# Kernel optimization log

Hardware: AMD Instinct MI355X
Metric: run time of the kernel (lower is better)

The kernel has to match this reference:

```python
import jax, jax.numpy as jnp
import numpy as np

WIDTH = 256
FREQS = 10
INPUT_WIDTH = 3 + 3 * 2 * FREQS  # 63


def embed_point(point, freqs):
    # point: [N, 3] -> [N, 3*(1+2*freqs)]
    linear = point[..., None]                                  # [N, 3, 1]
    scales = jnp.exp2(jnp.arange(freqs, dtype=point.dtype))    # [freqs]
    angles = linear * scales                                   # [N, 3, freqs]
    emb = jnp.concatenate((linear, jnp.sin(angles), jnp.cos(angles)), axis=-1)
    return emb.reshape(*point.shape[:-1], 3 * (1 + 2 * freqs))


def _xavier(key, fan_in, fan_out):
    limit = jnp.sqrt(6.0 / (fan_in + fan_out)).astype(jnp.float32)
    return jax.random.uniform(key, (fan_in, fan_out), jnp.float32, -limit, limit)


def setup_inputs() -> dict:
    key = jax.random.key(0)
    keys = jax.random.split(key, 20)
    N = 524288
    point = jax.random.normal(keys[0], (N, 3), dtype=jnp.float32)
    dims = [
        (INPUT_WIDTH, WIDTH), (WIDTH, WIDTH), (WIDTH, WIDTH), (WIDTH, WIDTH),
        (WIDTH, WIDTH), (WIDTH + INPUT_WIDTH, WIDTH), (WIDTH, WIDTH),
        (WIDTH, WIDTH), (WIDTH, 4),
    ]
    inp = {"point": point}
    for i, (fi, fo) in enumerate(dims):
        inp[f"w{i}"] = _xavier(keys[1 + i], fi, fo)
        inp[f"b{i}"] = jnp.zeros((fo,), dtype=jnp.float32)
    return inp


def reference(point, w0, b0, w1, b1, w2, b2, w3, b3, w4, b4,
              w5, b5, w6, b6, w7, b7, w8, b8):
    inp = embed_point(point, FREQS)                 # [N, 63]
    x = jax.nn.relu(inp @ w0 + b0)
    x = jax.nn.relu(x @ w1 + b1)
    x = jax.nn.relu(x @ w2 + b2)
    x = jax.nn.relu(x @ w3 + b3)
    x = jax.nn.relu(x @ w4 + b4)
    x = jax.nn.relu(jnp.concatenate((x, inp), -1) @ w5 + b5)  # skip concat
    x = jax.nn.relu(x @ w6 + b6)
    x = jax.nn.relu(x @ w7 + b7)
    return x @ w8 + b8                              # [N, 4]
```

## Files before the change

### kernel.cpp

```cpp
#include <hip/hip_runtime.h>
#include <math.h>


typedef __attribute__((ext_vector_type(8))) short short8;
typedef __attribute__((ext_vector_type(4))) float f32x4;

struct WPtrs { const float* w[8]; };
struct BPtrs { const float* b[8]; };

#define INV2PI 0.15915494309189533577f

#define ACT_PITCH 264
#define EMB_PITCH 72

#define PK_L0 0
#define PK_L1 16384
#define PK_L2 81920
#define PK_L3 147456
#define PK_L4 212992
#define PK_L5 278528
#define PK_L6 360448
#define PK_L7 425984
#define PK_W8 491520
#define PK_TOTAL 495616

__device__ __forceinline__ unsigned short f2bf(float v) {
  unsigned u = __float_as_uint(v);
  u = u + 0x7fffu + ((u >> 16) & 1u);
  return (unsigned short)(u >> 16);
}
__device__ __forceinline__ float bf_lo(unsigned u) { return __uint_as_float(u << 16); }
__device__ __forceinline__ float bf_hi(unsigned u) { return __uint_as_float(u & 0xffff0000u); }

__device__ __forceinline__ unsigned cvtpk(float a, float b) {
#if __has_builtin(__builtin_amdgcn_cvt_pk_bf16_f32)
  typedef __attribute__((ext_vector_type(2))) __bf16 bf16x2_t;
  bf16x2_t r = __builtin_amdgcn_cvt_pk_bf16_f32(a, b);
  return __builtin_bit_cast(unsigned, r);
#else
  unsigned ua = __float_as_uint(a);
  ua += 0x7fffu + ((ua >> 16) & 1u);
  unsigned ub = __float_as_uint(b);
  ub += 0x7fffu + ((ub >> 16) & 1u);
#if __has_builtin(__builtin_amdgcn_perm)
  return __builtin_amdgcn_perm(ub, ua, 0x07060302u);
#else
  return (ua >> 16) | (ub & 0xffff0000u);
#endif
#endif
}

__device__ __forceinline__ float fractf_(float x) {
#if __has_builtin(__builtin_amdgcn_fract_f32)
  return __builtin_amdgcn_fract_f32(x);
#else
  return x - floorf(x);
#endif
}
__device__ __forceinline__ float sin_rev(float rev) {
#if __has_builtin(__builtin_amdgcn_sinf)
  return __builtin_amdgcn_sinf(rev);
#else
  return __sinf(rev * 6.283185307179586f);
#endif
}

__device__ __forceinline__ float embval(int f, float c0, float c1, float c2,
                                        float x0, float x1, float x2) {
  if (f >= 63) return 0.0f;
  int d = (f >= 21 ? 1 : 0) + (f >= 42 ? 1 : 0);
  int r = f - d * 21;
  float c = (d == 0) ? c0 : (d == 1 ? c1 : c2);
  float x = (d == 0) ? x0 : (d == 1 ? x1 : x2);
  bool isc = r > 10;
  int e = isc ? (r - 11) : (r - 1);
  float rev = fractf_(ldexpf(x, e) + (isc ? 0.25f : 0.0f));
  float s = sin_rev(rev);
  return (r == 0) ? c : s;
}

__device__ __forceinline__ f32x4 mfma16(short8 a, short8 b, f32x4 c) {
  return __builtin_amdgcn_mfma_f32_16x16x32_bf16(a, b, c, 0, 0, 0);
}

__global__ void pack_weights(WPtrs W, const float* __restrict__ w8,
                             unsigned short* __restrict__ out) {
  int idx = blockIdx.x * 256 + threadIdx.x;
  if (idx >= PK_TOTAL) return;
  float v;
  if (idx >= PK_W8) {
    int t = idx - PK_W8;
    int j = t >> 8, k = t & 255;
    v = (j < 4) ? w8[k * 4 + j] : 0.0f;
  } else {
    int e = idx & 31;
    int blk = idx >> 5;
    int kkg = blk >> 8;
    int ch = blk & 255;
    int l, kk0;
    if      (kkg < 2)  { l = 0; kk0 = 0;  }
    else if (kkg < 10) { l = 1; kk0 = 2;  }
    else if (kkg < 18) { l = 2; kk0 = 10; }
    else if (kkg < 26) { l = 3; kk0 = 18; }
    else if (kkg < 34) { l = 4; kk0 = 26; }
    else if (kkg < 44) { l = 5; kk0 = 34; }
    else if (kkg < 52) { l = 6; kk0 = 44; }
    else               { l = 7; kk0 = 52; }
    int k = (kkg - kk0) * 32 + e;
    const int realK[8] = {63, 256, 256, 256, 256, 319, 256, 256};
    v = (k < realK[l]) ? W.w[l][k * 256 + ch] : 0.0f;
  }
  out[idx] = f2bf(v);
}

template <int KKA, int PA, int KKB, bool RB>
__device__ __forceinline__ void do_layer(
    const unsigned short* srcA, const unsigned short* srcB,
    const unsigned short* __restrict__ wblk,
    const float* __restrict__ bias,
    unsigned short* dst, int w, int quad, int l16) {
  f32x4 acc[4][4];
#pragma unroll
  for (int mt = 0; mt < 4; ++mt) {
    f32x4 bv = *reinterpret_cast<const f32x4*>(bias + w * 64 + mt * 16 + quad * 4);
#pragma unroll
    for (int nt = 0; nt < 4; ++nt) acc[mt][nt] = bv;
  }

  const unsigned short* ab = wblk + (unsigned)((w * 64 + l16) * 32 + quad * 8);
  const unsigned short* ba = srcA + (unsigned)(l16 * PA + quad * 8);

#pragma unroll 2
  for (int kk = 0; kk < KKA; ++kk) {
    short8 af[4];
#pragma unroll
    for (int mt = 0; mt < 4; ++mt)
      af[mt] = *reinterpret_cast<const short8*>(ab + mt * 512);
    ab += 8192;
    short8 bf[4];
#pragma unroll
    for (int nt = 0; nt < 4; ++nt)
      bf[nt] = *reinterpret_cast<const short8*>(ba + nt * 16 * PA);
    ba += 32;
#pragma unroll
    for (int mt = 0; mt < 4; ++mt)
#pragma unroll
      for (int nt = 0; nt < 4; ++nt)
        acc[mt][nt] = mfma16(af[mt], bf[nt], acc[mt][nt]);
  }
  if (KKB > 0) {
    const unsigned short* bb = srcB + (unsigned)(l16 * EMB_PITCH + quad * 8);
#pragma unroll
    for (int kk = 0; kk < KKB; ++kk) {
      short8 af[4];
#pragma unroll
      for (int mt = 0; mt < 4; ++mt)
        af[mt] = *reinterpret_cast<const short8*>(ab + mt * 512);
      ab += 8192;
      short8 bf[4];
#pragma unroll
      for (int nt = 0; nt < 4; ++nt)
        bf[nt] = *reinterpret_cast<const short8*>(bb + nt * 16 * EMB_PITCH);
      bb += 32;
#pragma unroll
      for (int mt = 0; mt < 4; ++mt)
#pragma unroll
        for (int nt = 0; nt < 4; ++nt)
          acc[mt][nt] = mfma16(af[mt], bf[nt], acc[mt][nt]);
    }
  }

  if (RB) __syncthreads();
#pragma unroll
  for (int nt = 0; nt < 4; ++nt) {
    unsigned short* rowp = dst + (unsigned)((nt * 16 + l16) * ACT_PITCH);
#pragma unroll
    for (int mt = 0; mt < 4; ++mt) {
      f32x4 v = acc[mt][nt];
      uint2 pr;
      pr.x = cvtpk(fmaxf(v.x, 0.0f), fmaxf(v.y, 0.0f));
      pr.y = cvtpk(fmaxf(v.z, 0.0f), fmaxf(v.w, 0.0f));
      *reinterpret_cast<uint2*>(rowp + (unsigned)(w * 64 + mt * 16 + quad * 4)) = pr;
    }
  }
  __syncthreads();
}

__launch_bounds__(256, 3)
__global__ void mlp_mfma(const float* __restrict__ pts, long N,
                         BPtrs B, const float* __restrict__ b8,
                         const unsigned short* __restrict__ wpk,
                         float* __restrict__ out) {
  __shared__ unsigned short act[64 * ACT_PITCH];
  __shared__ unsigned short emb[64 * EMB_PITCH];
  const int tid = threadIdx.x;
  const int w = tid >> 6, lane = tid & 63;
  const int quad = lane >> 4, l16 = lane & 15;
  const long pbase = (long)blockIdx.x * 64;

  {
    const int pt = tid >> 2, fg = tid & 3;
    const long pg = pbase + pt;
    float c0 = 0.f, c1 = 0.f, c2 = 0.f;
    if (pg < N) {
      const float* pp = pts + pg * 3;
      c0 = pp[0]; c1 = pp[1]; c2 = pp[2];
    }
    float x0 = c0 * INV2PI, x1 = c1 * INV2PI, x2 = c2 * INV2PI;
    unsigned pk[8];
#pragma unroll
    for (int i = 0; i < 16; i += 2) {
      int f0 = fg * 16 + i;
      float v0 = embval(f0,     c0, c1, c2, x0, x1, x2);
      float v1 = embval(f0 + 1, c0, c1, c2, x0, x1, x2);
      pk[i >> 1] = cvtpk(v0, v1);
    }
    uint4* dp = reinterpret_cast<uint4*>(emb + pt * EMB_PITCH + fg * 16);
    dp[0] = uint4{pk[0], pk[1], pk[2], pk[3]};
    dp[1] = uint4{pk[4], pk[5], pk[6], pk[7]};
  }
  __syncthreads();

  do_layer<2, EMB_PITCH, 0, false>(emb, nullptr, wpk + PK_L0, B.b[0], act, w, quad, l16);
  do_layer<8, ACT_PITCH, 0, true >(act, nullptr, wpk + PK_L1, B.b[1], act, w, quad, l16);
  do_layer<8, ACT_PITCH, 0, true >(act, nullptr, wpk + PK_L2, B.b[2], act, w, quad, l16);
  do_layer<8, ACT_PITCH, 0, true >(act, nullptr, wpk + PK_L3, B.b[3], act, w, quad, l16);
  do_layer<8, ACT_PITCH, 0, true >(act, nullptr, wpk + PK_L4, B.b[4], act, w, quad, l16);
  do_layer<8, ACT_PITCH, 2, true >(act, emb,     wpk + PK_L5, B.b[5], act, w, quad, l16);
  do_layer<8, ACT_PITCH, 0, true >(act, nullptr, wpk + PK_L6, B.b[6], act, w, quad, l16);
  do_layer<8, ACT_PITCH, 0, true >(act, nullptr, wpk + PK_L7, B.b[7], act, w, quad, l16);

  {
    const unsigned short* w8b = wpk + PK_W8 + (unsigned)(l16 * 256 + quad * 8);
    const unsigned short* ba = act + (unsigned)((w * 16 + l16) * ACT_PITCH + quad * 8);
    f32x4 acc = {0.f, 0.f, 0.f, 0.f};
#pragma unroll
    for (int kk = 0; kk < 8; ++kk) {
      short8 a = *reinterpret_cast<const short8*>(w8b + kk * 32);
      short8 b = *reinterpret_cast<const short8*>(ba + kk * 32);
      acc = mfma16(a, b, acc);
    }
    if (quad == 0) {
      f32x4 bb = *reinterpret_cast<const f32x4*>(b8);
      long pg = pbase + w * 16 + l16;
      f32x4 v = acc + bb;
      if (pg < N) *reinterpret_cast<f32x4*>(out + pg * 4) = v;
    }
  }
}

__device__ __forceinline__ unsigned pk2s(float a, float b) {
  return (unsigned)f2bf(a) | ((unsigned)f2bf(b) << 16);
}
__device__ __forceinline__ void fb_seg(const unsigned short* src, int kRows,
                                       const float* __restrict__ wr,
                                       int lane, int ps, float acc[4][16]) {
#pragma unroll 4
  for (int k = 0; k < kRows; ++k) {
    const float* p = wr + k * 256 + lane;
    float w0 = p[0], w1 = p[64], w2 = p[128], w3 = p[192];
    const uint4* xr = reinterpret_cast<const uint4*>(src + ((k << 6) + ps));
    uint4 q0 = xr[0], q1 = xr[1];
    float x[16];
    x[0] = bf_lo(q0.x);  x[1] = bf_hi(q0.x);  x[2] = bf_lo(q0.y);  x[3] = bf_hi(q0.y);
    x[4] = bf_lo(q0.z);  x[5] = bf_hi(q0.z);  x[6] = bf_lo(q0.w);  x[7] = bf_hi(q0.w);
    x[8] = bf_lo(q1.x);  x[9] = bf_hi(q1.x);  x[10] = bf_lo(q1.y); x[11] = bf_hi(q1.y);
    x[12] = bf_lo(q1.z); x[13] = bf_hi(q1.z); x[14] = bf_lo(q1.w); x[15] = bf_hi(q1.w);
#pragma unroll
    for (int pp = 0; pp < 16; ++pp) {
      acc[0][pp] = fmaf(w0, x[pp], acc[0][pp]);
      acc[1][pp] = fmaf(w1, x[pp], acc[1][pp]);
      acc[2][pp] = fmaf(w2, x[pp], acc[2][pp]);
      acc[3][pp] = fmaf(w3, x[pp], acc[3][pp]);
    }
  }
}
__device__ __forceinline__ void fb_layer(const unsigned short* srcA, int kA,
                                         const unsigned short* srcB, int kB,
                                         const float* wrA, const float* wrB,
                                         const float* bias,
                                         unsigned short* dst, int lane, int ps) {
  float acc[4][16];
#pragma unroll
  for (int jt = 0; jt < 4; ++jt) {
    float bb = bias[lane + (jt << 6)];
#pragma unroll
    for (int pp = 0; pp < 16; ++pp) acc[jt][pp] = bb;
  }
  fb_seg(srcA, kA, wrA, lane, ps, acc);
  if (srcB) fb_seg(srcB, kB, wrB, lane, ps, acc);
#pragma unroll
  for (int jt = 0; jt < 4; ++jt) {
    unsigned short* dr = dst + (((lane + (jt << 6)) << 6) + ps);
    float r[16];
#pragma unroll
    for (int pp = 0; pp < 16; ++pp) r[pp] = fmaxf(acc[jt][pp], 0.0f);
    uint4 a, b;
    a.x = pk2s(r[0], r[1]);   a.y = pk2s(r[2], r[3]);
    a.z = pk2s(r[4], r[5]);   a.w = pk2s(r[6], r[7]);
    b.x = pk2s(r[8], r[9]);   b.y = pk2s(r[10], r[11]);
    b.z = pk2s(r[12], r[13]); b.w = pk2s(r[14], r[15]);
    reinterpret_cast<uint4*>(dr)[0] = a;
    reinterpret_cast<uint4*>(dr)[1] = b;
  }
}
__launch_bounds__(256, 2)
__global__ void mlp_fallback(const float* __restrict__ pts, int N,
                             WPtrs W, BPtrs B,
                             const float* __restrict__ w8,
                             const float* __restrict__ b8,
                             float* __restrict__ out) {
  __shared__ unsigned short act[256 * 64];
  __shared__ unsigned short emb[64 * 64];
  const int lane = threadIdx.x & 63;
  const int ps = (threadIdx.x >> 6) << 4;
  const long pbase = (long)blockIdx.x * 64 + ps;
#pragma unroll
  for (int i = 0; i < 16; ++i) {
    int idx = (i << 6) + lane;
    int f = idx >> 4, pp = idx & 15;
    float v = 0.0f;
    if (f < 63) {
      float c = (pbase + pp < N) ? pts[(pbase + pp) * 3 + (f / 21)] : 0.0f;
      float x = c * INV2PI;
      v = embval(f, c, c, c, x, x, x);
    }
    emb[(f << 6) + ps + pp] = f2bf(v);
  }
  fb_layer(emb, 63, nullptr, 0, W.w[0], nullptr, B.b[0], act, lane, ps);
#pragma unroll 1
  for (int l = 1; l <= 4; ++l)
    fb_layer(act, 256, nullptr, 0, W.w[l], nullptr, B.b[l], act, lane, ps);
  fb_layer(act, 256, emb, 63, W.w[5], W.w[5] + 256 * 256, B.b[5], act, lane, ps);
#pragma unroll 1
  for (int l = 6; l <= 7; ++l)
    fb_layer(act, 256, nullptr, 0, W.w[l], nullptr, B.b[l], act, lane, ps);
  {
    const int pp = lane & 15, cc = lane >> 4;
    float a = b8[cc];
#pragma unroll 4
    for (int k = 0; k < 256; ++k)
      a = fmaf(bf_lo((unsigned)act[(k << 6) + ps + pp]), w8[(k << 2) + cc], a);
    if (pbase + pp < N) out[(pbase + pp) * 4 + cc] = a;
  }
}

extern "C" void kernel_launch(void* const* d_in, const int* in_sizes, int n_in,
                              void* d_out, int out_size, void* d_ws, size_t ws_size,
                              hipStream_t stream) {
  const float* pts = (const float*)d_in[0];
  WPtrs W; BPtrs B;
  for (int i = 0; i < 8; ++i) {
    W.w[i] = (const float*)d_in[1 + 2 * i];
    B.b[i] = (const float*)d_in[2 + 2 * i];
  }
  const float* w8 = (const float*)d_in[17];
  const float* b8 = (const float*)d_in[18];
  float* out = (float*)d_out;
  const long N = in_sizes[0] / 3;

  const size_t need = (size_t)PK_TOTAL * sizeof(unsigned short);
  if (ws_size >= need) {
    unsigned short* wpk = (unsigned short*)d_ws;
    pack_weights<<<1936, 256, 0, stream>>>(W, w8, wpk);
    mlp_mfma<<<(int)((N + 63) / 64), 256, 0, stream>>>(pts, N, B, b8, wpk, out);
  } else {
    mlp_fallback<<<(int)((N + 63) / 64), 256, 0, stream>>>(pts, (int)N, W, B, w8, b8, out);
  }
}
```

Baseline: 621.1 us.

## Switch MLP layers to 32x32x16 MFMA with XOR-swizzled LDS activations

Replaces the 16x16x32 bf16 MFMA tiling with the 32x32x16 instruction, giving each wave a 2x2 grid of 32x32 accumulators. The weight packing kernel is changed to match, using K-groups of 16. Padded LDS pitches are replaced by unpadded rows with an XOR swizzle so LDS reads and writes avoid bank conflicts. The smaller shared-memory footprint lets launch bounds rise from 3 to 4 blocks per CU, traded against register pressure from the larger accumulators.

```diff
diff --git a/kernel.cpp b/kernel.cpp
--- a/kernel.cpp
+++ b/kernel.cpp
@@ -4,14 +4,12 @@
 
 typedef __attribute__((ext_vector_type(8))) short short8;
 typedef __attribute__((ext_vector_type(4))) float f32x4;
+typedef __attribute__((ext_vector_type(16))) float f32x16;
 
 struct WPtrs { const float* w[8]; };
 struct BPtrs { const float* b[8]; };
 
 #define INV2PI 0.15915494309189533577f
-
-#define ACT_PITCH 264
-#define EMB_PITCH 72
 
 #define PK_L0 0
 #define PK_L1 16384
@@ -79,6 +77,9 @@
   return (r == 0) ? c : s;
 }
 
+__device__ __forceinline__ f32x16 mfma32(short8 a, short8 b, f32x16 c) {
+  return __builtin_amdgcn_mfma_f32_32x32x16_bf16(a, b, c, 0, 0, 0);
+}
 __device__ __forceinline__ f32x4 mfma16(short8 a, short8 b, f32x4 c) {
   return __builtin_amdgcn_mfma_f32_16x16x32_bf16(a, b, c, 0, 0, 0);
 }
@@ -93,109 +94,112 @@
     int j = t >> 8, k = t & 255;
     v = (j < 4) ? w8[k * 4 + j] : 0.0f;
   } else {
-    int e = idx & 31;
-    int blk = idx >> 5;
+    int e = idx & 15;
+    int blk = idx >> 4;
+    int ch = blk & 255;
     int kkg = blk >> 8;
-    int ch = blk & 255;
     int l, kk0;
-    if      (kkg < 2)  { l = 0; kk0 = 0;  }
-    else if (kkg < 10) { l = 1; kk0 = 2;  }
-    else if (kkg < 18) { l = 2; kk0 = 10; }
-    else if (kkg < 26) { l = 3; kk0 = 18; }
-    else if (kkg < 34) { l = 4; kk0 = 26; }
-    else if (kkg < 44) { l = 5; kk0 = 34; }
-    else if (kkg < 52) { l = 6; kk0 = 44; }
-    else               { l = 7; kk0 = 52; }
-    int k = (kkg - kk0) * 32 + e;
+    if      (kkg < 4)   { l = 0; kk0 = 0;   }
+    else if (kkg < 20)  { l = 1; kk0 = 4;   }
+    else if (kkg < 36)  { l = 2; kk0 = 20;  }
+    else if (kkg < 52)  { l = 3; kk0 = 36;  }
+    else if (kkg < 68)  { l = 4; kk0 = 52;  }
+    else if (kkg < 88)  { l = 5; kk0 = 68;  }
+    else if (kkg < 104) { l = 6; kk0 = 88;  }
+    else                { l = 7; kk0 = 104; }
+    int k = (kkg - kk0) * 16 + e;
     const int realK[8] = {63, 256, 256, 256, 256, 319, 256, 256};
     v = (k < realK[l]) ? W.w[l][k * 256 + ch] : 0.0f;
   }
   out[idx] = f2bf(v);
 }
 
-template <int KKA, int PA, int KKB, bool RB>
-__device__ __forceinline__ void do_layer(
+template <int KKA, int PAB, int KKB, bool RB>
+__device__ __forceinline__ void do_layer32(
     const unsigned short* srcA, const unsigned short* srcB,
     const unsigned short* __restrict__ wblk,
     const float* __restrict__ bias,
-    unsigned short* dst, int w, int quad, int l16) {
-  f32x4 acc[4][4];
-#pragma unroll
-  for (int mt = 0; mt < 4; ++mt) {
-    f32x4 bv = *reinterpret_cast<const f32x4*>(bias + w * 64 + mt * 16 + quad * 4);
-#pragma unroll
-    for (int nt = 0; nt < 4; ++nt) acc[mt][nt] = bv;
-  }
-
-  const unsigned short* ab = wblk + (unsigned)((w * 64 + l16) * 32 + quad * 8);
-  const unsigned short* ba = srcA + (unsigned)(l16 * PA + quad * 8);
-
-#pragma unroll 2
+    unsigned short* dst, int w, int n, int h, unsigned swz) {
+  f32x16 acc[2][2];
+#pragma unroll
+  for (int mt = 0; mt < 2; ++mt)
+#pragma unroll
+    for (int q = 0; q < 4; ++q) {
+      f32x4 bq = *reinterpret_cast<const f32x4*>(bias + w * 64 + mt * 32 + q * 8 + h * 4);
+#pragma unroll
+      for (int r = 0; r < 4; ++r) {
+        acc[mt][0][q * 4 + r] = bq[r];
+        acc[mt][1][q * 4 + r] = bq[r];
+      }
+    }
+
+  const unsigned short* ab = wblk + (unsigned)((w * 64 + n) * 16 + h * 8);
+  const char* rA0 = (const char*)srcA + (unsigned)(n * PAB);
+  const char* rA1 = rA0 + 32 * PAB;
+
+#pragma unroll 4
   for (int kk = 0; kk < KKA; ++kk) {
-    short8 af[4];
-#pragma unroll
-    for (int mt = 0; mt < 4; ++mt)
-      af[mt] = *reinterpret_cast<const short8*>(ab + mt * 512);
-    ab += 8192;
-    short8 bf[4];
-#pragma unroll
-    for (int nt = 0; nt < 4; ++nt)
-      bf[nt] = *reinterpret_cast<const short8*>(ba + nt * 16 * PA);
-    ba += 32;
-#pragma unroll
-    for (int mt = 0; mt < 4; ++mt)
-#pragma unroll
-      for (int nt = 0; nt < 4; ++nt)
-        acc[mt][nt] = mfma16(af[mt], bf[nt], acc[mt][nt]);
+    short8 a0 = *reinterpret_cast<const short8*>(ab + kk * 4096);
+    short8 a1 = *reinterpret_cast<const short8*>(ab + kk * 4096 + 512);
+    unsigned off = ((unsigned)(kk * 32 + h * 16)) ^ swz;
+    short8 b0 = *reinterpret_cast<const short8*>(rA0 + off);
+    short8 b1 = *reinterpret_cast<const short8*>(rA1 + off);
+    acc[0][0] = mfma32(a0, b0, acc[0][0]);
+    acc[0][1] = mfma32(a0, b1, acc[0][1]);
+    acc[1][0] = mfma32(a1, b0, acc[1][0]);
+    acc[1][1] = mfma32(a1, b1, acc[1][1]);
   }
   if (KKB > 0) {
-    const unsigned short* bb = srcB + (unsigned)(l16 * EMB_PITCH + quad * 8);
-#pragma unroll
-    for (int kk = 0; kk < KKB; ++kk) {
-      short8 af[4];
-#pragma unroll
-      for (int mt = 0; mt < 4; ++mt)
-        af[mt] = *reinterpret_cast<const short8*>(ab + mt * 512);
-      ab += 8192;
-      short8 bf[4];
-#pragma unroll
-      for (int nt = 0; nt < 4; ++nt)
-        bf[nt] = *reinterpret_cast<const short8*>(bb + nt * 16 * EMB_PITCH);
-      bb += 32;
-#pragma unroll
-      for (int mt = 0; mt < 4; ++mt)
-#pragma unroll
-        for (int nt = 0; nt < 4; ++nt)
-          acc[mt][nt] = mfma16(af[mt], bf[nt], acc[mt][nt]);
+    const char* rB0 = (const char*)srcB + (unsigned)(n * 128);
+    const char* rB1 = rB0 + 32 * 128;
+#pragma unroll
+    for (int kl = 0; kl < KKB; ++kl) {
+      const unsigned short* ab2 = ab + (KKA + kl) * 4096;
+      short8 a0 = *reinterpret_cast<const short8*>(ab2);
+      short8 a1 = *reinterpret_cast<const short8*>(ab2 + 512);
+      unsigned off = ((unsigned)(kl * 32 + h * 16)) ^ swz;
+      short8 b0 = *reinterpret_cast<const short8*>(rB0 + off);
+      short8 b1 = *reinterpret_cast<const short8*>(rB1 + off);
+      acc[0][0] = mfma32(a0, b0, acc[0][0]);
+      acc[0][1] = mfma32(a0, b1, acc[0][1]);
+      acc[1][0] = mfma32(a1, b0, acc[1][0]);
+      acc[1][1] = mfma32(a1, b1, acc[1][1]);
     }
   }
 
   if (RB) __syncthreads();
 #pragma unroll
-  for (int nt = 0; nt < 4; ++nt) {
-    unsigned short* rowp = dst + (unsigned)((nt * 16 + l16) * ACT_PITCH);
-#pragma unroll
-    for (int mt = 0; mt < 4; ++mt) {
-      f32x4 v = acc[mt][nt];
-      uint2 pr;
-      pr.x = cvtpk(fmaxf(v.x, 0.0f), fmaxf(v.y, 0.0f));
-      pr.y = cvtpk(fmaxf(v.z, 0.0f), fmaxf(v.w, 0.0f));
-      *reinterpret_cast<uint2*>(rowp + (unsigned)(w * 64 + mt * 16 + quad * 4)) = pr;
-    }
+  for (int nt = 0; nt < 2; ++nt) {
+    char* rowp = (char*)dst + (unsigned)((nt * 32 + n) * 512);
+#pragma unroll
+    for (int mt = 0; mt < 2; ++mt)
+#pragma unroll
+      for (int q = 0; q < 4; ++q) {
+        float x0 = fmaxf(acc[mt][nt][q * 4 + 0], 0.0f);
+        float x1 = fmaxf(acc[mt][nt][q * 4 + 1], 0.0f);
+        float x2 = fmaxf(acc[mt][nt][q * 4 + 2], 0.0f);
+        float x3 = fmaxf(acc[mt][nt][q * 4 + 3], 0.0f);
+        uint2 pr;
+        pr.x = cvtpk(x0, x1);
+        pr.y = cvtpk(x2, x3);
+        unsigned off = ((unsigned)(w * 128 + mt * 64 + q * 16 + h * 8)) ^ swz;
+        *reinterpret_cast<uint2*>(rowp + off) = pr;
+      }
   }
   __syncthreads();
 }
 
-__launch_bounds__(256, 3)
+__launch_bounds__(256, 4)
 __global__ void mlp_mfma(const float* __restrict__ pts, long N,
                          BPtrs B, const float* __restrict__ b8,
                          const unsigned short* __restrict__ wpk,
                          float* __restrict__ out) {
-  __shared__ unsigned short act[64 * ACT_PITCH];
-  __shared__ unsigned short emb[64 * EMB_PITCH];
+  __shared__ unsigned short act[64 * 256];
+  __shared__ unsigned short emb[64 * 64];
   const int tid = threadIdx.x;
   const int w = tid >> 6, lane = tid & 63;
-  const int quad = lane >> 4, l16 = lane & 15;
+  const int n = lane & 31, h = lane >> 5;
+  const unsigned swz = (unsigned)((n & 7) << 4);
   const long pbase = (long)blockIdx.x * 64;
 
   {
@@ -215,35 +219,41 @@
       float v1 = embval(f0 + 1, c0, c1, c2, x0, x1, x2);
       pk[i >> 1] = cvtpk(v0, v1);
     }
-    uint4* dp = reinterpret_cast<uint4*>(emb + pt * EMB_PITCH + fg * 16);
-    dp[0] = uint4{pk[0], pk[1], pk[2], pk[3]};
-    dp[1] = uint4{pk[4], pk[5], pk[6], pk[7]};
+    const unsigned sw = (unsigned)((pt & 7) << 4);
+    char* rowp = (char*)emb + (unsigned)(pt * 128);
+    *reinterpret_cast<uint4*>(rowp + (((unsigned)(fg * 32)) ^ sw)) =
+        uint4{pk[0], pk[1], pk[2], pk[3]};
+    *reinterpret_cast<uint4*>(rowp + (((unsigned)(fg * 32 + 16)) ^ sw)) =
+        uint4{pk[4], pk[5], pk[6], pk[7]};
   }
   __syncthreads();
 
-  do_layer<2, EMB_PITCH, 0, false>(emb, nullptr, wpk + PK_L0, B.b[0], act, w, quad, l16);
-  do_layer<8, ACT_PITCH, 0, true >(act, nullptr, wpk + PK_L1, B.b[1], act, w, quad, l16);
-  do_layer<8, ACT_PITCH, 0, true >(act, nullptr, wpk + PK_L2, B.b[2], act, w, quad, l16);
-  do_layer<8, ACT_PITCH, 0, true >(act, nullptr, wpk + PK_L3, B.b[3], act, w, quad, l16);
-  do_layer<8, ACT_PITCH, 0, true >(act, nullptr, wpk + PK_L4, B.b[4], act, w, quad, l16);
-  do_layer<8, ACT_PITCH, 2, true >(act, emb,     wpk + PK_L5, B.b[5], act, w, quad, l16);
-  do_layer<8, ACT_PITCH, 0, true >(act, nullptr, wpk + PK_L6, B.b[6], act, w, quad, l16);
-  do_layer<8, ACT_PITCH, 0, true >(act, nullptr, wpk + PK_L7, B.b[7], act, w, quad, l16);
+  do_layer32<4,  128, 0, false>(emb, nullptr, wpk + PK_L0, B.b[0], act, w, n, h, swz);
+  do_layer32<16, 512, 0, true >(act, nullptr, wpk + PK_L1, B.b[1], act, w, n, h, swz);
+  do_layer32<16, 512, 0, true >(act, nullptr, wpk + PK_L2, B.b[2], act, w, n, h, swz);
+  do_layer32<16, 512, 0, true >(act, nullptr, wpk + PK_L3, B.b[3], act, w, n, h, swz);
+  do_layer32<16, 512, 0, true >(act, nullptr, wpk + PK_L4, B.b[4], act, w, n, h, swz);
+  do_layer32<16, 512, 4, true >(act, emb,     wpk + PK_L5, B.b[5], act, w, n, h, swz);
+  do_layer32<16, 512, 0, true >(act, nullptr, wpk + PK_L6, B.b[6], act, w, n, h, swz);
+  do_layer32<16, 512, 0, true >(act, nullptr, wpk + PK_L7, B.b[7], act, w, n, h, swz);
 
   {
+    const int l16 = lane & 15, quad = lane >> 4;
     const unsigned short* w8b = wpk + PK_W8 + (unsigned)(l16 * 256 + quad * 8);
-    const unsigned short* ba = act + (unsigned)((w * 16 + l16) * ACT_PITCH + quad * 8);
-    f32x4 acc = {0.f, 0.f, 0.f, 0.f};
+    const int pt = w * 16 + l16;
+    const char* ba = (const char*)act + (unsigned)(pt * 512);
+    f32x4 a4 = {0.f, 0.f, 0.f, 0.f};
 #pragma unroll
     for (int kk = 0; kk < 8; ++kk) {
       short8 a = *reinterpret_cast<const short8*>(w8b + kk * 32);
-      short8 b = *reinterpret_cast<const short8*>(ba + kk * 32);
-      acc = mfma16(a, b, acc);
+      unsigned off = ((unsigned)(kk * 64 + quad * 16)) ^ swz;
+      short8 b = *reinterpret_cast<const short8*>(ba + off);
+      a4 = mfma16(a, b, a4);
     }
     if (quad == 0) {
       f32x4 bb = *reinterpret_cast<const f32x4*>(b8);
-      long pg = pbase + w * 16 + l16;
-      f32x4 v = acc + bb;
+      long pg = pbase + pt;
+      f32x4 v = a4 + bb;
       if (pg < N) *reinterpret_cast<f32x4*>(out + pg * 4) = v;
     }
   }
```

After: 602.9 us. -2.9%, faster.
